# Performance work log

Measured on AMD Instinct MI355X. Metric: run time of the kernel, lower is better.

Reference implementation:

```python
import jax, jax.numpy as jnp
import numpy as np

B, T, N = 16, 1000, 100
ENC, VOCAB, EMB, HID, ATT, PROJ = 512, 10025, 640, 1024, 1024, 1024


def setup_inputs() -> dict:
    key = jax.random.key(0)
    ks = jax.random.split(key, 20)
    g = lambda k, shape, s=0.02: (jax.random.normal(k, shape) * s).astype(jnp.float32)
    inp = {
        "encoder_outputs": jax.random.normal(ks[0], (B, T, ENC), dtype=jnp.float32),
        "labels": jax.random.randint(ks[1], (B, N), 0, VOCAB),
        "enc_seq_len": jax.random.randint(ks[2], (B,), T // 2, T + 1),
        # parameters (torch layout: Linear weight [out, in])
        "embed_table": g(ks[3], (VOCAB, EMB)),
        "W_ih": g(ks[4], (4 * HID, EMB + ENC)),
        "W_hh": g(ks[5], (4 * HID, HID)),
        "b_ih": jnp.zeros((4 * HID,), jnp.float32),
        "b_hh": jnp.zeros((4 * HID,), jnp.float32),
        "W_s": g(ks[6], (ATT, HID)),              # s_transformed, no bias
        "W_enc": g(ks[7], (ATT, ENC)),            # enc_ctx
        "b_enc": jnp.zeros((ATT,), jnp.float32),
        "v_att": g(ks[8], (ATT,)),                # attention energy vector
        "W_fert": g(ks[9], (ENC,)),               # inv_fertility [1,ENC] squeezed
        "W_fb": g(ks[10], (ATT,)),                # weight_feedback [ATT,1] squeezed
        "W_ro": g(ks[11], (PROJ, HID + EMB + ENC)),
        "b_ro": jnp.zeros((PROJ,), jnp.float32),
        "W_out": g(ks[12], (VOCAB, PROJ // 2)),
        "b_out": jnp.zeros((VOCAB,), jnp.float32),
    }
    return inp


def _decode(encoder_outputs, labels, enc_seq_len, embed_table, W_ih, W_hh, b_ih,
            b_hh, W_s, W_enc, b_enc, v_att, W_fert, W_fb, W_ro, b_ro, W_out, b_out):
    Bb, Tt, _ = encoder_outputs.shape
    # shifted target embeddings: pad one zero step at front, drop last -> [B,N,EMB]
    emb = embed_table[labels]
    emb = jnp.concatenate([jnp.zeros_like(emb[:, :1]), emb[:, :-1]], axis=1)

    enc_ctx = jnp.einsum("btd,ad->bta", encoder_outputs, W_enc) + b_enc  # [B,T,ATT]
    inv_fert = jax.nn.sigmoid(encoder_outputs @ W_fert)                   # [B,T]
    seq_mask = jnp.arange(Tt)[None, :] < enc_seq_len[:, None]             # [B,T]

    def step(carry, e_t):
        h, c, att_ctx, accum = carry  # h,c:[B,HID]  att_ctx:[B,ENC]  accum:[B,T]
        x = jnp.concatenate([e_t, att_ctx], axis=-1)
        gates = x @ W_ih.T + b_ih + h @ W_hh.T + b_hh
        i, f, gg, o = jnp.split(gates, 4, axis=-1)
        c_new = jax.nn.sigmoid(f) * c + jax.nn.sigmoid(i) * jnp.tanh(gg)
        h_new = jax.nn.sigmoid(o) * jnp.tanh(c_new)

        s_t = h_new @ W_s.T                                   # [B,ATT]
        wf = accum[:, :, None] * W_fb[None, None, :]          # [B,T,ATT]
        energies = jnp.tanh(enc_ctx + s_t[:, None, :] + wf) @ v_att  # [B,T]
        energies = jnp.where(seq_mask, energies, -jnp.inf)
        weights = jax.nn.softmax(energies, axis=1)            # [B,T]
        ctx = jnp.einsum("bt,btd->bd", weights, encoder_outputs)
        accum_new = accum + weights * inv_fert * 0.5
        return (h_new, c_new, ctx, accum_new), (h_new, ctx)

    carry0 = (
        jnp.zeros((Bb, HID), jnp.float32),
        jnp.zeros((Bb, HID), jnp.float32),
        jnp.zeros((Bb, ENC), jnp.float32),
        jnp.zeros((Bb, Tt), jnp.float32),
    )
    carry, (s_seq, ctx_seq) = jax.lax.scan(step, carry0, emb.transpose(1, 0, 2))
    s_stacked = s_seq.transpose(1, 0, 2)        # [B,N,HID]
    ctx_stacked = ctx_seq.transpose(1, 0, 2)    # [B,N,ENC]

    ro_in = jnp.concatenate([s_stacked, emb, ctx_stacked], axis=-1) @ W_ro.T + b_ro
    readout = jnp.max(ro_in.reshape(Bb, ro_in.shape[1], -1, 2), axis=-1)  # maxout
    logits = readout @ W_out.T + b_out
    return logits, carry


def reference(encoder_outputs, labels, enc_seq_len, embed_table, W_ih, W_hh, b_ih,
              b_hh, W_s, W_enc, b_enc, v_att, W_fert, W_fb, W_ro, b_ro, W_out, b_out):
    logits, (h, c, att_ctx, accum) = _decode(
        encoder_outputs, labels, enc_seq_len, embed_table, W_ih, W_hh, b_ih, b_hh,
        W_s, W_enc, b_enc, v_att, W_fert, W_fb, W_ro, b_ro, W_out, b_out)
    return logits, h, c, att_ctx, accum
```

## Files before the change

kernel.cpp:

```cpp
#include <hip/hip_runtime.h>
#include <math.h>

#define Bsz 16
#define Tsz 1000
#define Nsz 100
#define ENC 512
#define VOCAB 10025
#define EMB 640
#define HID 1024
#define ATT 1024
#define KX (EMB + ENC)
#define KRO (HID + EMB + ENC)

typedef short s16x8 __attribute__((ext_vector_type(8)));
typedef unsigned short u16x4 __attribute__((ext_vector_type(4)));
typedef float f32x4 __attribute__((ext_vector_type(4)));

__device__ __forceinline__ float4 ld4(const float* p) { return *reinterpret_cast<const float4*>(p); }
__device__ __forceinline__ float dot4(float4 a, float4 b) { return a.x*b.x + a.y*b.y + a.z*b.z + a.w*b.w; }
__device__ __forceinline__ float sigmoidf_(float x) { return 1.f / (1.f + __expf(-x)); }
__device__ __forceinline__ float ftanh_(float x) {
    x = fminf(15.f, fmaxf(-15.f, x));
    float e = __expf(2.f * x);
    return (e - 1.f) / (e + 1.f);
}
__device__ __forceinline__ unsigned short f2bf(float x) {
    union { float f; unsigned u; } v; v.f = x;
    unsigned r = v.u + 0x7fffu + ((v.u >> 16) & 1u);
    return (unsigned short)(r >> 16);
}
__device__ __forceinline__ float bf2f(unsigned short h) {
    union { float f; unsigned u; } v; v.u = ((unsigned)h) << 16;
    return v.f;
}

__global__ __launch_bounds__(256) void k_init(float* accum) {
    int i = blockIdx.x * 256 + threadIdx.x;
    if (i < Bsz * Tsz) accum[i] = 0.f;
}

__global__ __launch_bounds__(256) void k_embed(const int* __restrict__ labels,
                                               const float* __restrict__ table,
                                               float* __restrict__ roA) {
    int idx = blockIdx.x * 256 + threadIdx.x;
    if (idx >= Bsz * Nsz * EMB) return;
    int e = idx % EMB;
    int bn = idx / EMB;
    int n = bn % Nsz, b = bn / Nsz;
    float v = 0.f;
    if (n > 0) {
        int lab = labels[b * Nsz + n - 1];
        v = table[(size_t)lab * EMB + e];
    }
    roA[(size_t)bn * KRO + HID + e] = v;
}

template <int MODE>
__global__ __launch_bounds__(256) void mfma_gemm(const float* __restrict__ A,
                                                 const float* __restrict__ W,
                                                 const float* __restrict__ bias,
                                                 float* __restrict__ C,
                                                 int M, int Nc, int K, int ldC) {
    __shared__ unsigned short Ah[128][40], Al[128][40], Wh[128][40], Wl[128][40];
    int tid = threadIdx.x;
    int lane = tid & 63;
    int wave = tid >> 6;
    int wm = (wave >> 1) * 64, wn = (wave & 1) * 64;
    int m0 = blockIdx.y * 128, n0 = blockIdx.x * 128;
    int lrow = tid >> 1;
    int lcol = (tid & 1) * 16;
    bool aval = (m0 + lrow) < M;
    bool wval = (n0 + lrow) < Nc;
    const float* Arow = A + (size_t)(m0 + lrow) * K + lcol;
    const float* Wrow = W + (size_t)(n0 + lrow) * K + lcol;
    int frow = lane & 15, fk = (lane >> 4) * 8;

    f32x4 acc[4][4];
#pragma unroll
    for (int i = 0; i < 4; i++)
#pragma unroll
        for (int j = 0; j < 4; j++) acc[i][j] = (f32x4){0.f, 0.f, 0.f, 0.f};

    const float4 z4 = {0.f, 0.f, 0.f, 0.f};
    for (int k0 = 0; k0 < K; k0 += 32) {
#pragma unroll
        for (int c = 0; c < 16; c += 4) {
            float4 av = aval ? ld4(Arow + k0 + c) : z4;
            u16x4 hv, lv;
            hv.x = f2bf(av.x); lv.x = f2bf(av.x - bf2f(hv.x));
            hv.y = f2bf(av.y); lv.y = f2bf(av.y - bf2f(hv.y));
            hv.z = f2bf(av.z); lv.z = f2bf(av.z - bf2f(hv.z));
            hv.w = f2bf(av.w); lv.w = f2bf(av.w - bf2f(hv.w));
            *(u16x4*)&Ah[lrow][lcol + c] = hv;
            *(u16x4*)&Al[lrow][lcol + c] = lv;
            float4 wv = wval ? ld4(Wrow + k0 + c) : z4;
            hv.x = f2bf(wv.x); lv.x = f2bf(wv.x - bf2f(hv.x));
            hv.y = f2bf(wv.y); lv.y = f2bf(wv.y - bf2f(hv.y));
            hv.z = f2bf(wv.z); lv.z = f2bf(wv.z - bf2f(hv.z));
            hv.w = f2bf(wv.w); lv.w = f2bf(wv.w - bf2f(hv.w));
            *(u16x4*)&Wh[lrow][lcol + c] = hv;
            *(u16x4*)&Wl[lrow][lcol + c] = lv;
        }
        __syncthreads();
        s16x8 afh[4], afl[4], bfh[4], bfl[4];
#pragma unroll
        for (int i = 0; i < 4; i++) {
            afh[i] = *(const s16x8*)&Ah[wm + i * 16 + frow][fk];
            afl[i] = *(const s16x8*)&Al[wm + i * 16 + frow][fk];
            bfh[i] = *(const s16x8*)&Wh[wn + i * 16 + frow][fk];
            bfl[i] = *(const s16x8*)&Wl[wn + i * 16 + frow][fk];
        }
#pragma unroll
        for (int mi = 0; mi < 4; mi++)
#pragma unroll
            for (int ni = 0; ni < 4; ni++) {
                acc[mi][ni] = __builtin_amdgcn_mfma_f32_16x16x32_bf16(afh[mi], bfh[ni], acc[mi][ni], 0, 0, 0);
                acc[mi][ni] = __builtin_amdgcn_mfma_f32_16x16x32_bf16(afl[mi], bfh[ni], acc[mi][ni], 0, 0, 0);
                acc[mi][ni] = __builtin_amdgcn_mfma_f32_16x16x32_bf16(afh[mi], bfl[ni], acc[mi][ni], 0, 0, 0);
            }
        __syncthreads();
    }
    int crb = (lane >> 4) * 4;
    int ccol = lane & 15;
#pragma unroll
    for (int mi = 0; mi < 4; mi++) {
#pragma unroll
        for (int r = 0; r < 4; r++) {
            int m = m0 + wm + mi * 16 + crb + r;
#pragma unroll
            for (int ni = 0; ni < 4; ni++) {
                int n = n0 + wn + ni * 16 + ccol;
                if (MODE == 0) {
                    if (m < M && n < Nc) C[(size_t)m * ldC + n] = acc[mi][ni][r] + bias[n];
                } else {
                    float v = (n < Nc) ? acc[mi][ni][r] + bias[n] : -INFINITY;
                    float o = __shfl_xor(v, 1, 64);
                    if (((lane & 1) == 0) && m < M && n < Nc)
                        C[(size_t)m * ldC + (n >> 1)] = fmaxf(v, o);
                }
            }
        }
    }
}

__global__ __launch_bounds__(256) void k_ifert(const float* __restrict__ enc,
                                               const float* __restrict__ Wfert,
                                               float* __restrict__ ifert) {
    int wv = (blockIdx.x * 256 + threadIdx.x) >> 6;
    int lane = threadIdx.x & 63;
    if (wv >= Bsz * Tsz) return;
    const float* row = enc + (size_t)wv * ENC;
    float s = 0.f;
    for (int k = lane * 4; k < ENC; k += 256) s += dot4(ld4(row + k), ld4(Wfert + k));
    for (int o = 32; o; o >>= 1) s += __shfl_xor(s, o, 64);
    if (lane == 0) ifert[wv] = 1.f / (1.f + __expf(-s));
}

__global__ __launch_bounds__(256) void k_gates(float* __restrict__ roA, float* __restrict__ cbuf,
                                               const float* __restrict__ Wih, const float* __restrict__ Whh,
                                               const float* __restrict__ bih, const float* __restrict__ bhh,
                                               int t) {
    int wv = (blockIdx.x * 256 + threadIdx.x) >> 6;
    int lane = threadIdx.x & 63;
    int j = wv >> 1;
    int b0 = (wv & 1) << 3;
    float acc[4][8];
#pragma unroll
    for (int g = 0; g < 4; g++)
#pragma unroll
        for (int bb = 0; bb < 8; bb++) acc[g][bb] = 0.f;

    const float* wi0 = Wih + (size_t)(0 * HID + j) * KX;
    const float* wi1 = Wih + (size_t)(1 * HID + j) * KX;
    const float* wi2 = Wih + (size_t)(2 * HID + j) * KX;
    const float* wi3 = Wih + (size_t)(3 * HID + j) * KX;
    const float* wh0 = Whh + (size_t)(0 * HID + j) * HID;
    const float* wh1 = Whh + (size_t)(1 * HID + j) * HID;
    const float* wh2 = Whh + (size_t)(2 * HID + j) * HID;
    const float* wh3 = Whh + (size_t)(3 * HID + j) * HID;
    const float* xrow[8];
    const float* prow[8];
#pragma unroll
    for (int bb = 0; bb < 8; bb++) {
        xrow[bb] = roA + (size_t)((b0 + bb) * Nsz + t) * KRO;
        prow[bb] = roA + (size_t)((b0 + bb) * Nsz + (t - 1)) * KRO;
    }
    for (int k = lane * 4; k < EMB; k += 256) {
        float4 w0 = ld4(wi0 + k), w1 = ld4(wi1 + k), w2 = ld4(wi2 + k), w3 = ld4(wi3 + k);
#pragma unroll
        for (int bb = 0; bb < 8; bb++) {
            float4 x = ld4(xrow[bb] + HID + k);
            acc[0][bb] += dot4(w0, x); acc[1][bb] += dot4(w1, x);
            acc[2][bb] += dot4(w2, x); acc[3][bb] += dot4(w3, x);
        }
    }
    if (t > 0) {
        for (int k = lane * 4; k < ENC; k += 256) {
            float4 w0 = ld4(wi0 + EMB + k), w1 = ld4(wi1 + EMB + k), w2 = ld4(wi2 + EMB + k), w3 = ld4(wi3 + EMB + k);
#pragma unroll
            for (int bb = 0; bb < 8; bb++) {
                float4 x = ld4(prow[bb] + HID + EMB + k);
                acc[0][bb] += dot4(w0, x); acc[1][bb] += dot4(w1, x);
                acc[2][bb] += dot4(w2, x); acc[3][bb] += dot4(w3, x);
            }
        }
        for (int k = lane * 4; k < HID; k += 256) {
            float4 w0 = ld4(wh0 + k), w1 = ld4(wh1 + k), w2 = ld4(wh2 + k), w3 = ld4(wh3 + k);
#pragma unroll
            for (int bb = 0; bb < 8; bb++) {
                float4 x = ld4(prow[bb] + k);
                acc[0][bb] += dot4(w0, x); acc[1][bb] += dot4(w1, x);
                acc[2][bb] += dot4(w2, x); acc[3][bb] += dot4(w3, x);
            }
        }
    }
#pragma unroll
    for (int g = 0; g < 4; g++)
#pragma unroll
        for (int bb = 0; bb < 8; bb++) {
            float v = acc[g][bb];
            for (int o = 32; o; o >>= 1) v += __shfl_xor(v, o, 64);
            acc[g][bb] = v;
        }
    if (lane < 8) {
        int b = b0 + lane;
        float gi = acc[0][lane] + bih[j] + bhh[j];
        float gf = acc[1][lane] + bih[HID + j] + bhh[HID + j];
        float gg = acc[2][lane] + bih[2 * HID + j] + bhh[2 * HID + j];
        float go = acc[3][lane] + bih[3 * HID + j] + bhh[3 * HID + j];
        float cold = (t > 0) ? cbuf[b * HID + j] : 0.f;
        float cn = sigmoidf_(gf) * cold + sigmoidf_(gi) * ftanh_(gg);
        float hn = sigmoidf_(go) * ftanh_(cn);
        cbuf[b * HID + j] = cn;
        roA[(size_t)(b * Nsz + t) * KRO + j] = hn;
    }
}

__global__ __launch_bounds__(256) void k_s(const float* __restrict__ roA, const float* __restrict__ Wsm,
                                           float* __restrict__ st, int t) {
    int wv = (blockIdx.x * 256 + threadIdx.x) >> 6;
    int lane = threadIdx.x & 63;
    float acc[16];
#pragma unroll
    for (int b = 0; b < 16; b++) acc[b] = 0.f;
    const float* wr = Wsm + (size_t)wv * HID;
    const float* hrow[16];
#pragma unroll
    for (int b = 0; b < 16; b++) hrow[b] = roA + (size_t)(b * Nsz + t) * KRO;
    for (int k = lane * 4; k < HID; k += 256) {
        float4 w = ld4(wr + k);
#pragma unroll
        for (int b = 0; b < 16; b++) acc[b] += dot4(w, ld4(hrow[b] + k));
    }
#pragma unroll
    for (int b = 0; b < 16; b++) {
        float v = acc[b];
        for (int o = 32; o; o >>= 1) v += __shfl_xor(v, o, 64);
        acc[b] = v;
    }
    if (lane < 16) st[lane * ATT + wv] = acc[lane];
}

__global__ __launch_bounds__(256) void k_energy(const float* __restrict__ encctx,
                                                const float* __restrict__ st,
                                                const float* __restrict__ Wfb,
                                                const float* __restrict__ vatt,
                                                const float* __restrict__ accum,
                                                const int* __restrict__ seqlen,
                                                float* __restrict__ enw) {
    int wv = (blockIdx.x * 256 + threadIdx.x) >> 6;
    int lane = threadIdx.x & 63;
    int b = wv / Tsz, t = wv - b * Tsz;
    if (t >= seqlen[b]) {
        if (lane == 0) enw[wv] = -INFINITY;
        return;
    }
    float ac = accum[wv];
    const float* ec = encctx + (size_t)wv * ATT;
    const float* sr = st + b * ATT;
    float e = 0.f;
    for (int k = lane * 4; k < ATT; k += 256) {
        float4 c4 = ld4(ec + k), s4 = ld4(sr + k), f4 = ld4(Wfb + k), v4 = ld4(vatt + k);
        e += ftanh_(c4.x + s4.x + ac * f4.x) * v4.x;
        e += ftanh_(c4.y + s4.y + ac * f4.y) * v4.y;
        e += ftanh_(c4.z + s4.z + ac * f4.z) * v4.z;
        e += ftanh_(c4.w + s4.w + ac * f4.w) * v4.w;
    }
    for (int o = 32; o; o >>= 1) e += __shfl_xor(e, o, 64);
    if (lane == 0) enw[wv] = e;
}

__global__ __launch_bounds__(256) void k_softmax(float* __restrict__ enw, const float* __restrict__ ifert,
                                                 float* __restrict__ accum, float* __restrict__ roA,
                                                 const int* __restrict__ seqlen, int tstep) {
    int b = blockIdx.x, tid = threadIdx.x;
    __shared__ float redm[4], reds[4];
    int len = seqlen[b];
    float* row = enw + b * Tsz;
    float m = -INFINITY;
    for (int t = tid; t < len; t += 256) m = fmaxf(m, row[t]);
    for (int o = 32; o; o >>= 1) m = fmaxf(m, __shfl_xor(m, o, 64));
    if ((tid & 63) == 0) redm[tid >> 6] = m;
    __syncthreads();
    float M = fmaxf(fmaxf(redm[0], redm[1]), fmaxf(redm[2], redm[3]));
    float s = 0.f;
    for (int t = tid; t < len; t += 256) s += __expf(row[t] - M);
    for (int o = 32; o; o >>= 1) s += __shfl_xor(s, o, 64);
    if ((tid & 63) == 0) reds[tid >> 6] = s;
    __syncthreads();
    float inv = 1.f / (reds[0] + reds[1] + reds[2] + reds[3]);
    for (int t = tid; t < Tsz; t += 256) {
        float w = (t < len) ? __expf(row[t] - M) * inv : 0.f;
        row[t] = w;
        accum[b * Tsz + t] += w * ifert[b * Tsz + t] * 0.5f;
    }
    for (int d = tid; d < ENC; d += 256) roA[(size_t)(b * Nsz + tstep) * KRO + HID + EMB + d] = 0.f;
}

#define TCH 10
__global__ __launch_bounds__(256) void k_ctx(const float* __restrict__ enw, const float* __restrict__ enc,
                                             const int* __restrict__ seqlen, float* __restrict__ roA,
                                             int tstep) {
    int b = blockIdx.y;
    int tid = threadIdx.x;
    int len = seqlen[b];
    int t0 = blockIdx.x * (Tsz / TCH);
    int t1 = min(t0 + Tsz / TCH, len);
    if (t0 >= t1) return;
    float a0 = 0.f, a1 = 0.f;
    const float* w = enw + b * Tsz;
    for (int t = t0; t < t1; t++) {
        float wt = w[t];
        const float* er = enc + (size_t)(b * Tsz + t) * ENC;
        a0 += wt * er[tid];
        a1 += wt * er[tid + 256];
    }
    float* dst = roA + (size_t)(b * Nsz + tstep) * KRO + HID + EMB;
    atomicAdd(dst + tid, a0);
    atomicAdd(dst + tid + 256, a1);
}

__global__ __launch_bounds__(256) void k_final(const float* __restrict__ roA, const float* __restrict__ cbuf,
                                               const float* __restrict__ accum, float* __restrict__ out) {
    int idx = blockIdx.x * 256 + threadIdx.x;
    const int base = Bsz * Nsz * VOCAB;
    const int OH = Bsz * HID, OC = Bsz * HID, OA = Bsz * ENC, OAC = Bsz * Tsz;
    if (idx < OH) {
        int b = idx / HID, j = idx % HID;
        out[base + idx] = roA[(size_t)(b * Nsz + Nsz - 1) * KRO + j];
        return;
    }
    idx -= OH;
    if (idx < OC) { out[base + OH + idx] = cbuf[idx]; return; }
    idx -= OC;
    if (idx < OA) {
        int b = idx / ENC, d = idx % ENC;
        out[base + OH + OC + idx] = roA[(size_t)(b * Nsz + Nsz - 1) * KRO + HID + EMB + d];
        return;
    }
    idx -= OA;
    if (idx < OAC) out[base + OH + OC + OA + idx] = accum[idx];
}

extern "C" void kernel_launch(void* const* d_in, const int* in_sizes, int n_in,
                              void* d_out, int out_size, void* d_ws, size_t ws_size,
                              hipStream_t stream) {
    const float* enc   = (const float*)d_in[0];
    const int* labels  = (const int*)d_in[1];
    const int* seqlen  = (const int*)d_in[2];
    const float* table = (const float*)d_in[3];
    const float* Wih   = (const float*)d_in[4];
    const float* Whh   = (const float*)d_in[5];
    const float* bih   = (const float*)d_in[6];
    const float* bhh   = (const float*)d_in[7];
    const float* Wsm   = (const float*)d_in[8];
    const float* Wenc  = (const float*)d_in[9];
    const float* benc  = (const float*)d_in[10];
    const float* vatt  = (const float*)d_in[11];
    const float* Wfert = (const float*)d_in[12];
    const float* Wfb   = (const float*)d_in[13];
    const float* Wro   = (const float*)d_in[14];
    const float* bro   = (const float*)d_in[15];
    const float* Wout  = (const float*)d_in[16];
    const float* bout  = (const float*)d_in[17];
    float* out = (float*)d_out;

    float* ws = (float*)d_ws;
    float* roA    = ws;
    float* cbuf   = roA + (size_t)1600 * KRO;
    float* encctx = cbuf + Bsz * HID;
    float* ifert  = encctx + (size_t)Bsz * Tsz * ATT;
    float* accum  = ifert + Bsz * Tsz;
    float* enw    = accum + Bsz * Tsz;
    float* st     = enw + Bsz * Tsz;
    float* rmx    = st + Bsz * ATT;

    k_init<<<(Bsz * Tsz + 255) / 256, 256, 0, stream>>>(accum);
    k_embed<<<(Bsz * Nsz * EMB + 255) / 256, 256, 0, stream>>>(labels, table, roA);
    mfma_gemm<0><<<dim3(ATT / 128, (Bsz * Tsz) / 128), 256, 0, stream>>>(enc, Wenc, benc, encctx,
                                                                        Bsz * Tsz, ATT, ENC, ATT);
    k_ifert<<<(Bsz * Tsz * 64 + 255) / 256, 256, 0, stream>>>(enc, Wfert, ifert);

    for (int t = 0; t < Nsz; t++) {
        k_gates<<<512, 256, 0, stream>>>(roA, cbuf, Wih, Whh, bih, bhh, t);
        k_s<<<256, 256, 0, stream>>>(roA, Wsm, st, t);
        k_energy<<<(Bsz * Tsz * 64) / 256, 256, 0, stream>>>(encctx, st, Wfb, vatt, accum, seqlen, enw);
        k_softmax<<<Bsz, 256, 0, stream>>>(enw, ifert, accum, roA, seqlen, t);
        k_ctx<<<dim3(TCH, Bsz), 256, 0, stream>>>(enw, enc, seqlen, roA, t);
    }

    mfma_gemm<1><<<dim3(1024 / 128, (1600 + 127) / 128), 256, 0, stream>>>(roA, Wro, bro, rmx,
                                                                          1600, 1024, KRO, 512);
    mfma_gemm<0><<<dim3((VOCAB + 127) / 128, (1600 + 127) / 128), 256, 0, stream>>>(rmx, Wout, bout, out,
                                                                                   1600, VOCAB, 512, VOCAB);
    k_final<<<(Bsz * HID * 2 + Bsz * ENC + Bsz * Tsz + 255) / 256, 256, 0, stream>>>(roA, cbuf, accum, out);
}
```

Baseline: 7.996 ms.

## Hoist embedding gate GEMM out of loop, store enc_ctx in bf16, fuse softmax with context

The embedding part of the LSTM input projection (plus summed biases) is precomputed for all steps with one MFMA GEMM before the recurrence. The per-step gate kernel then only handles the attention-context and hidden-state terms, covering all 16 batches per wave. The attention projection enc_ctx is stored as bf16, halving the bandwidth the energy kernel reads each step. Softmax and context accumulation are fused into one kernel, and context zeroing moves into the energy kernel, removing one launch per step. The costs are reduced precision in the attention energies and the softmax being recomputed in each chunk block.

```diff
diff --git a/kernel.cpp b/kernel.cpp
--- a/kernel.cpp
+++ b/kernel.cpp
@@ -11,9 +11,11 @@
 #define ATT 1024
 #define KX (EMB + ENC)
 #define KRO (HID + EMB + ENC)
+#define G4 (4 * HID)
 
 typedef short s16x8 __attribute__((ext_vector_type(8)));
 typedef unsigned short u16x4 __attribute__((ext_vector_type(4)));
+typedef unsigned short u16x8 __attribute__((ext_vector_type(8)));
 typedef float f32x4 __attribute__((ext_vector_type(4)));
 
 __device__ __forceinline__ float4 ld4(const float* p) { return *reinterpret_cast<const float4*>(p); }
@@ -34,9 +36,11 @@
     return v.f;
 }
 
-__global__ __launch_bounds__(256) void k_init(float* accum) {
+__global__ __launch_bounds__(256) void k_init(float* accum, const float* __restrict__ bih,
+                                              const float* __restrict__ bhh, float* __restrict__ bsum) {
     int i = blockIdx.x * 256 + threadIdx.x;
     if (i < Bsz * Tsz) accum[i] = 0.f;
+    if (i < G4) bsum[i] = bih[i] + bhh[i];
 }
 
 __global__ __launch_bounds__(256) void k_embed(const int* __restrict__ labels,
@@ -56,8 +60,8 @@
 }
 
 template <int MODE>
-__global__ __launch_bounds__(256) void mfma_gemm(const float* __restrict__ A,
-                                                 const float* __restrict__ W,
+__global__ __launch_bounds__(256) void mfma_gemm(const float* __restrict__ A, int lda,
+                                                 const float* __restrict__ W, int ldw,
                                                  const float* __restrict__ bias,
                                                  float* __restrict__ C,
                                                  int M, int Nc, int K, int ldC) {
@@ -71,8 +75,8 @@
     int lcol = (tid & 1) * 16;
     bool aval = (m0 + lrow) < M;
     bool wval = (n0 + lrow) < Nc;
-    const float* Arow = A + (size_t)(m0 + lrow) * K + lcol;
-    const float* Wrow = W + (size_t)(n0 + lrow) * K + lcol;
+    const float* Arow = A + (size_t)(m0 + lrow) * lda + lcol;
+    const float* Wrow = W + (size_t)(n0 + lrow) * ldw + lcol;
     int frow = lane & 15, fk = (lane >> 4) * 8;
 
     f32x4 acc[4][4];
@@ -132,6 +136,9 @@
                 int n = n0 + wn + ni * 16 + ccol;
                 if (MODE == 0) {
                     if (m < M && n < Nc) C[(size_t)m * ldC + n] = acc[mi][ni][r] + bias[n];
+                } else if (MODE == 2) {
+                    if (m < M && n < Nc)
+                        ((unsigned short*)C)[(size_t)m * ldC + n] = f2bf(acc[mi][ni][r] + bias[n]);
                 } else {
                     float v = (n < Nc) ? acc[mi][ni][r] + bias[n] : -INFINITY;
                     float o = __shfl_xor(v, 1, 64);
@@ -156,78 +163,63 @@
     if (lane == 0) ifert[wv] = 1.f / (1.f + __expf(-s));
 }
 
-__global__ __launch_bounds__(256) void k_gates(float* __restrict__ roA, float* __restrict__ cbuf,
-                                               const float* __restrict__ Wih, const float* __restrict__ Whh,
-                                               const float* __restrict__ bih, const float* __restrict__ bhh,
-                                               int t) {
-    int wv = (blockIdx.x * 256 + threadIdx.x) >> 6;
+__global__ __launch_bounds__(256) void k_gates2(float* __restrict__ roA, float* __restrict__ cbuf,
+                                                const float* __restrict__ gpre,
+                                                const float* __restrict__ Wih, const float* __restrict__ Whh,
+                                                int t) {
+    __shared__ float red[4][4][16];
     int lane = threadIdx.x & 63;
-    int j = wv >> 1;
-    int b0 = (wv & 1) << 3;
-    float acc[4][8];
+    int wid = threadIdx.x >> 6;
+    int j = blockIdx.x * 4 + wid;
+    float acc[4][16];
 #pragma unroll
     for (int g = 0; g < 4; g++)
 #pragma unroll
-        for (int bb = 0; bb < 8; bb++) acc[g][bb] = 0.f;
-
-    const float* wi0 = Wih + (size_t)(0 * HID + j) * KX;
-    const float* wi1 = Wih + (size_t)(1 * HID + j) * KX;
-    const float* wi2 = Wih + (size_t)(2 * HID + j) * KX;
-    const float* wi3 = Wih + (size_t)(3 * HID + j) * KX;
-    const float* wh0 = Whh + (size_t)(0 * HID + j) * HID;
-    const float* wh1 = Whh + (size_t)(1 * HID + j) * HID;
-    const float* wh2 = Whh + (size_t)(2 * HID + j) * HID;
-    const float* wh3 = Whh + (size_t)(3 * HID + j) * HID;
-    const float* xrow[8];
-    const float* prow[8];
-#pragma unroll
-    for (int bb = 0; bb < 8; bb++) {
-        xrow[bb] = roA + (size_t)((b0 + bb) * Nsz + t) * KRO;
-        prow[bb] = roA + (size_t)((b0 + bb) * Nsz + (t - 1)) * KRO;
-    }
-    for (int k = lane * 4; k < EMB; k += 256) {
-        float4 w0 = ld4(wi0 + k), w1 = ld4(wi1 + k), w2 = ld4(wi2 + k), w3 = ld4(wi3 + k);
-#pragma unroll
-        for (int bb = 0; bb < 8; bb++) {
-            float4 x = ld4(xrow[bb] + HID + k);
-            acc[0][bb] += dot4(w0, x); acc[1][bb] += dot4(w1, x);
-            acc[2][bb] += dot4(w2, x); acc[3][bb] += dot4(w3, x);
-        }
-    }
+        for (int b = 0; b < 16; b++) acc[g][b] = 0.f;
     if (t > 0) {
+        const float* wc0 = Wih + (size_t)(0 * HID + j) * KX + EMB;
+        const float* wc1 = Wih + (size_t)(1 * HID + j) * KX + EMB;
+        const float* wc2 = Wih + (size_t)(2 * HID + j) * KX + EMB;
+        const float* wc3 = Wih + (size_t)(3 * HID + j) * KX + EMB;
+        const float* wh0 = Whh + (size_t)(0 * HID + j) * HID;
+        const float* wh1 = Whh + (size_t)(1 * HID + j) * HID;
+        const float* wh2 = Whh + (size_t)(2 * HID + j) * HID;
+        const float* wh3 = Whh + (size_t)(3 * HID + j) * HID;
         for (int k = lane * 4; k < ENC; k += 256) {
-            float4 w0 = ld4(wi0 + EMB + k), w1 = ld4(wi1 + EMB + k), w2 = ld4(wi2 + EMB + k), w3 = ld4(wi3 + EMB + k);
-#pragma unroll
-            for (int bb = 0; bb < 8; bb++) {
-                float4 x = ld4(prow[bb] + HID + EMB + k);
-                acc[0][bb] += dot4(w0, x); acc[1][bb] += dot4(w1, x);
-                acc[2][bb] += dot4(w2, x); acc[3][bb] += dot4(w3, x);
+            float4 w0 = ld4(wc0 + k), w1 = ld4(wc1 + k), w2 = ld4(wc2 + k), w3 = ld4(wc3 + k);
+#pragma unroll
+            for (int b = 0; b < 16; b++) {
+                float4 x = ld4(&roA[(size_t)(b * Nsz + t - 1) * KRO + HID + EMB + k]);
+                acc[0][b] += dot4(w0, x); acc[1][b] += dot4(w1, x);
+                acc[2][b] += dot4(w2, x); acc[3][b] += dot4(w3, x);
             }
         }
         for (int k = lane * 4; k < HID; k += 256) {
             float4 w0 = ld4(wh0 + k), w1 = ld4(wh1 + k), w2 = ld4(wh2 + k), w3 = ld4(wh3 + k);
 #pragma unroll
-            for (int bb = 0; bb < 8; bb++) {
-                float4 x = ld4(prow[bb] + k);
-                acc[0][bb] += dot4(w0, x); acc[1][bb] += dot4(w1, x);
-                acc[2][bb] += dot4(w2, x); acc[3][bb] += dot4(w3, x);
+            for (int b = 0; b < 16; b++) {
+                float4 x = ld4(&roA[(size_t)(b * Nsz + t - 1) * KRO + k]);
+                acc[0][b] += dot4(w0, x); acc[1][b] += dot4(w1, x);
+                acc[2][b] += dot4(w2, x); acc[3][b] += dot4(w3, x);
             }
         }
     }
 #pragma unroll
     for (int g = 0; g < 4; g++)
 #pragma unroll
-        for (int bb = 0; bb < 8; bb++) {
-            float v = acc[g][bb];
+        for (int b = 0; b < 16; b++) {
+            float v = acc[g][b];
             for (int o = 32; o; o >>= 1) v += __shfl_xor(v, o, 64);
-            acc[g][bb] = v;
-        }
-    if (lane < 8) {
-        int b = b0 + lane;
-        float gi = acc[0][lane] + bih[j] + bhh[j];
-        float gf = acc[1][lane] + bih[HID + j] + bhh[HID + j];
-        float gg = acc[2][lane] + bih[2 * HID + j] + bhh[2 * HID + j];
-        float go = acc[3][lane] + bih[3 * HID + j] + bhh[3 * HID + j];
+            if (lane == 0) red[wid][g][b] = v;
+        }
+    __syncthreads();
+    if (lane < 16) {
+        int b = lane;
+        const float* gp = gpre + (size_t)(b * Nsz + t) * G4 + j;
+        float gi = red[wid][0][b] + gp[0];
+        float gf = red[wid][1][b] + gp[HID];
+        float gg = red[wid][2][b] + gp[2 * HID];
+        float go = red[wid][3][b] + gp[3 * HID];
         float cold = (t > 0) ? cbuf[b * HID + j] : 0.f;
         float cn = sigmoidf_(gf) * cold + sigmoidf_(gi) * ftanh_(gg);
         float hn = sigmoidf_(go) * ftanh_(cn);
@@ -244,13 +236,10 @@
 #pragma unroll
     for (int b = 0; b < 16; b++) acc[b] = 0.f;
     const float* wr = Wsm + (size_t)wv * HID;
-    const float* hrow[16];
-#pragma unroll
-    for (int b = 0; b < 16; b++) hrow[b] = roA + (size_t)(b * Nsz + t) * KRO;
     for (int k = lane * 4; k < HID; k += 256) {
         float4 w = ld4(wr + k);
 #pragma unroll
-        for (int b = 0; b < 16; b++) acc[b] += dot4(w, ld4(hrow[b] + k));
+        for (int b = 0; b < 16; b++) acc[b] += dot4(w, ld4(&roA[(size_t)(b * Nsz + t) * KRO + k]));
     }
 #pragma unroll
     for (int b = 0; b < 16; b++) {
@@ -261,13 +250,19 @@
     if (lane < 16) st[lane * ATT + wv] = acc[lane];
 }
 
-__global__ __launch_bounds__(256) void k_energy(const float* __restrict__ encctx,
+__global__ __launch_bounds__(256) void k_energy(const unsigned short* __restrict__ encctx,
                                                 const float* __restrict__ st,
                                                 const float* __restrict__ Wfb,
                                                 const float* __restrict__ vatt,
                                                 const float* __restrict__ accum,
                                                 const int* __restrict__ seqlen,
-                                                float* __restrict__ enw) {
+                                                float* __restrict__ enw,
+                                                float* __restrict__ roA, int tstep) {
+    if (blockIdx.x < Bsz) {
+        float* dst = roA + (size_t)(blockIdx.x * Nsz + tstep) * KRO + HID + EMB;
+        dst[threadIdx.x] = 0.f;
+        dst[threadIdx.x + 256] = 0.f;
+    }
     int wv = (blockIdx.x * 256 + threadIdx.x) >> 6;
     int lane = threadIdx.x & 63;
     int b = wv / Tsz, t = wv - b * Tsz;
@@ -276,64 +271,61 @@
         return;
     }
     float ac = accum[wv];
-    const float* ec = encctx + (size_t)wv * ATT;
+    const unsigned short* ec = encctx + (size_t)wv * ATT;
     const float* sr = st + b * ATT;
     float e = 0.f;
-    for (int k = lane * 4; k < ATT; k += 256) {
-        float4 c4 = ld4(ec + k), s4 = ld4(sr + k), f4 = ld4(Wfb + k), v4 = ld4(vatt + k);
-        e += ftanh_(c4.x + s4.x + ac * f4.x) * v4.x;
-        e += ftanh_(c4.y + s4.y + ac * f4.y) * v4.y;
-        e += ftanh_(c4.z + s4.z + ac * f4.z) * v4.z;
-        e += ftanh_(c4.w + s4.w + ac * f4.w) * v4.w;
+    for (int k = lane * 8; k < ATT; k += 512) {
+        u16x8 c8 = *(const u16x8*)(ec + k);
+        float4 sa = ld4(sr + k), sb = ld4(sr + k + 4);
+        float4 fa = ld4(Wfb + k), fb = ld4(Wfb + k + 4);
+        float4 va = ld4(vatt + k), vb = ld4(vatt + k + 4);
+        e += ftanh_(bf2f(c8[0]) + sa.x + ac * fa.x) * va.x;
+        e += ftanh_(bf2f(c8[1]) + sa.y + ac * fa.y) * va.y;
+        e += ftanh_(bf2f(c8[2]) + sa.z + ac * fa.z) * va.z;
+        e += ftanh_(bf2f(c8[3]) + sa.w + ac * fa.w) * va.w;
+        e += ftanh_(bf2f(c8[4]) + sb.x + ac * fb.x) * vb.x;
+        e += ftanh_(bf2f(c8[5]) + sb.y + ac * fb.y) * vb.y;
+        e += ftanh_(bf2f(c8[6]) + sb.z + ac * fb.z) * vb.z;
+        e += ftanh_(bf2f(c8[7]) + sb.w + ac * fb.w) * vb.w;
     }
     for (int o = 32; o; o >>= 1) e += __shfl_xor(e, o, 64);
     if (lane == 0) enw[wv] = e;
 }
 
-__global__ __launch_bounds__(256) void k_softmax(float* __restrict__ enw, const float* __restrict__ ifert,
-                                                 float* __restrict__ accum, float* __restrict__ roA,
-                                                 const int* __restrict__ seqlen, int tstep) {
-    int b = blockIdx.x, tid = threadIdx.x;
+#define TCH 10
+__global__ __launch_bounds__(256) void k_softctx(const float* __restrict__ enw,
+                                                 const float* __restrict__ ifert,
+                                                 float* __restrict__ accum,
+                                                 const float* __restrict__ enc,
+                                                 const int* __restrict__ seqlen,
+                                                 float* __restrict__ roA, int tstep) {
+    int b = blockIdx.y, tid = threadIdx.x;
     __shared__ float redm[4], reds[4];
     int len = seqlen[b];
-    float* row = enw + b * Tsz;
+    const float* row = enw + b * Tsz;
     float m = -INFINITY;
-    for (int t = tid; t < len; t += 256) m = fmaxf(m, row[t]);
+    for (int i = tid; i < len; i += 256) m = fmaxf(m, row[i]);
     for (int o = 32; o; o >>= 1) m = fmaxf(m, __shfl_xor(m, o, 64));
     if ((tid & 63) == 0) redm[tid >> 6] = m;
     __syncthreads();
     float M = fmaxf(fmaxf(redm[0], redm[1]), fmaxf(redm[2], redm[3]));
     float s = 0.f;
-    for (int t = tid; t < len; t += 256) s += __expf(row[t] - M);
+    for (int i = tid; i < len; i += 256) s += __expf(row[i] - M);
     for (int o = 32; o; o >>= 1) s += __shfl_xor(s, o, 64);
     if ((tid & 63) == 0) reds[tid >> 6] = s;
     __syncthreads();
     float inv = 1.f / (reds[0] + reds[1] + reds[2] + reds[3]);
-    for (int t = tid; t < Tsz; t += 256) {
-        float w = (t < len) ? __expf(row[t] - M) * inv : 0.f;
-        row[t] = w;
-        accum[b * Tsz + t] += w * ifert[b * Tsz + t] * 0.5f;
-    }
-    for (int d = tid; d < ENC; d += 256) roA[(size_t)(b * Nsz + tstep) * KRO + HID + EMB + d] = 0.f;
-}
-
-#define TCH 10
-__global__ __launch_bounds__(256) void k_ctx(const float* __restrict__ enw, const float* __restrict__ enc,
-                                             const int* __restrict__ seqlen, float* __restrict__ roA,
-                                             int tstep) {
-    int b = blockIdx.y;
-    int tid = threadIdx.x;
-    int len = seqlen[b];
     int t0 = blockIdx.x * (Tsz / TCH);
     int t1 = min(t0 + Tsz / TCH, len);
+    for (int i = t0 + tid; i < t1; i += 256)
+        accum[b * Tsz + i] += __expf(row[i] - M) * inv * ifert[b * Tsz + i] * 0.5f;
     if (t0 >= t1) return;
     float a0 = 0.f, a1 = 0.f;
-    const float* w = enw + b * Tsz;
-    for (int t = t0; t < t1; t++) {
-        float wt = w[t];
-        const float* er = enc + (size_t)(b * Tsz + t) * ENC;
-        a0 += wt * er[tid];
-        a1 += wt * er[tid + 256];
+    for (int i = t0; i < t1; i++) {
+        float w = __expf(row[i] - M) * inv;
+        const float* er = enc + (size_t)(b * Tsz + i) * ENC;
+        a0 += w * er[tid];
+        a1 += w * er[tid + 256];
     }
     float* dst = roA + (size_t)(b * Nsz + tstep) * KRO + HID + EMB;
     atomicAdd(dst + tid, a0);
@@ -386,32 +378,37 @@
     float* out = (float*)d_out;
 
     float* ws = (float*)d_ws;
-    float* roA    = ws;
-    float* cbuf   = roA + (size_t)1600 * KRO;
-    float* encctx = cbuf + Bsz * HID;
-    float* ifert  = encctx + (size_t)Bsz * Tsz * ATT;
-    float* accum  = ifert + Bsz * Tsz;
-    float* enw    = accum + Bsz * Tsz;
-    float* st     = enw + Bsz * Tsz;
-    float* rmx    = st + Bsz * ATT;
-
-    k_init<<<(Bsz * Tsz + 255) / 256, 256, 0, stream>>>(accum);
+    float* roA  = ws;
+    float* cbuf = roA + (size_t)1600 * KRO;
+    float* gpre = cbuf + Bsz * HID;
+    unsigned short* encctx = (unsigned short*)(gpre + (size_t)1600 * G4);
+    float* after = gpre + (size_t)1600 * G4 + (size_t)Bsz * Tsz * ATT / 2;
+    float* ifert = after;
+    float* accum = ifert + Bsz * Tsz;
+    float* enw   = accum + Bsz * Tsz;
+    float* st    = enw + Bsz * Tsz;
+    float* bsum  = st + Bsz * ATT;
+    float* rmx   = bsum + G4;
+
+    k_init<<<(Bsz * Tsz + 255) / 256, 256, 0, stream>>>(accum, bih, bhh, bsum);
     k_embed<<<(Bsz * Nsz * EMB + 255) / 256, 256, 0, stream>>>(labels, table, roA);
-    mfma_gemm<0><<<dim3(ATT / 128, (Bsz * Tsz) / 128), 256, 0, stream>>>(enc, Wenc, benc, encctx,
-                                                                        Bsz * Tsz, ATT, ENC, ATT);
+    mfma_gemm<0><<<dim3(G4 / 128, (1600 + 127) / 128), 256, 0, stream>>>(
+        roA + HID, KRO, Wih, KX, bsum, gpre, 1600, G4, EMB, G4);
+    mfma_gemm<2><<<dim3(ATT / 128, (Bsz * Tsz) / 128), 256, 0, stream>>>(
+        enc, ENC, Wenc, ENC, benc, (float*)encctx, Bsz * Tsz, ATT, ENC, ATT);
     k_ifert<<<(Bsz * Tsz * 64 + 255) / 256, 256, 0, stream>>>(enc, Wfert, ifert);
 
     for (int t = 0; t < Nsz; t++) {
-        k_gates<<<512, 256, 0, stream>>>(roA, cbuf, Wih, Whh, bih, bhh, t);
+        k_gates2<<<256, 256, 0, stream>>>(roA, cbuf, gpre, Wih, Whh, t);
         k_s<<<256, 256, 0, stream>>>(roA, Wsm, st, t);
-        k_energy<<<(Bsz * Tsz * 64) / 256, 256, 0, stream>>>(encctx, st, Wfb, vatt, accum, seqlen, enw);
-        k_softmax<<<Bsz, 256, 0, stream>>>(enw, ifert, accum, roA, seqlen, t);
-        k_ctx<<<dim3(TCH, Bsz), 256, 0, stream>>>(enw, enc, seqlen, roA, t);
-    }
-
-    mfma_gemm<1><<<dim3(1024 / 128, (1600 + 127) / 128), 256, 0, stream>>>(roA, Wro, bro, rmx,
-                                                                          1600, 1024, KRO, 512);
-    mfma_gemm<0><<<dim3((VOCAB + 127) / 128, (1600 + 127) / 128), 256, 0, stream>>>(rmx, Wout, bout, out,
-                                                                                   1600, VOCAB, 512, VOCAB);
+        k_energy<<<(Bsz * Tsz * 64) / 256, 256, 0, stream>>>(encctx, st, Wfb, vatt, accum, seqlen,
+                                                             enw, roA, t);
+        k_softctx<<<dim3(TCH, Bsz), 256, 0, stream>>>(enw, ifert, accum, enc, seqlen, roA, t);
+    }
+
+    mfma_gemm<1><<<dim3(1024 / 128, (1600 + 127) / 128), 256, 0, stream>>>(
+        roA, KRO, Wro, KRO, bro, rmx, 1600, 1024, KRO, 512);
+    mfma_gemm<0><<<dim3((VOCAB + 127) / 128, (1600 + 127) / 128), 256, 0, stream>>>(
+        rmx, 512, Wout, 512, bout, out, 1600, VOCAB, 512, VOCAB);
     k_final<<<(Bsz * HID * 2 + Bsz * ENC + Bsz * Tsz + 255) / 256, 256, 0, stream>>>(roA, cbuf, accum, out);
 }
```

Measured after the change: 9.156 ms. 14.5% more time.
